# Kernel optimization log

Measured on AMD Instinct MI355X. Metric: run time of the kernel, lower is better.

The kernel has to match this reference:

```python
import jax, jax.numpy as jnp
import numpy as np

ELEM, EMBD, WIN = 128, 128, 128

def setup_inputs() -> dict:
    key = jax.random.key(0)
    ks = jax.random.split(key, 7)
    s = 1.0 / np.sqrt(ELEM)
    return {
        "x": jax.random.normal(ks[0], (8, 16384, ELEM), dtype=jnp.float32),
        "Wq": jax.random.uniform(ks[1], (EMBD, ELEM), jnp.float32, -s, s),
        "bq": jax.random.uniform(ks[2], (EMBD,), jnp.float32, -s, s),
        "Wk": jax.random.uniform(ks[3], (EMBD, ELEM), jnp.float32, -s, s),
        "bk": jax.random.uniform(ks[4], (EMBD,), jnp.float32, -s, s),
        "Wv": jax.random.uniform(ks[5], (EMBD, ELEM), jnp.float32, -s, s),
        "bv": jax.random.uniform(ks[6], (EMBD,), jnp.float32, -s, s),
    }

def reference(x, Wq, bq, Wk, bk, Wv, bv):
    N, S, E = x.shape
    P = S // WIN
    xp = x.reshape(N, P, WIN, E)  # [N,P,W,E]
    q = jnp.einsum('npwe,de->npwd', xp, Wq) + bq
    k = jnp.einsum('npwe,de->npwd', xp, Wk) + bk
    v = jnp.einsum('npwe,de->npwd', xp, Wv) + bv
    # note: original applies NO 1/sqrt(d) scaling
    scores = jnp.einsum('npwd,npud->npwu', q, k)  # [N,P,W,W]
    attn = jax.nn.softmax(scores, axis=-1)
    out = jnp.einsum('npwu,npud->npwd', attn, v)
    return out.reshape(N, S, EMBD)
```

## Files before the change

kernel.cpp:

```cpp
#include <hip/hip_runtime.h>

#define LDSP 136

typedef _Float16 h8 __attribute__((ext_vector_type(8)));
typedef _Float16 h4 __attribute__((ext_vector_type(4)));
typedef float    f4 __attribute__((ext_vector_type(4)));

__global__ void prep(const float* __restrict__ Wq, const float* __restrict__ Wk,
                     const float* __restrict__ bq, _Float16* __restrict__ Mt,
                     float* __restrict__ ck) {
    int idx = blockIdx.x * 256 + threadIdx.x;
    int e = idx & 127, f = idx >> 7;
    float a0 = 0.f, a1 = 0.f, a2 = 0.f, a3 = 0.f;
    for (int d = 0; d < 128; d += 4) {
        a0 += Wk[(d + 0) * 128 + f] * Wq[(d + 0) * 128 + e];
        a1 += Wk[(d + 1) * 128 + f] * Wq[(d + 1) * 128 + e];
        a2 += Wk[(d + 2) * 128 + f] * Wq[(d + 2) * 128 + e];
        a3 += Wk[(d + 3) * 128 + f] * Wq[(d + 3) * 128 + e];
    }
    Mt[idx] = (_Float16)((a0 + a1) + (a2 + a3));

    if (blockIdx.x == 0 && threadIdx.x < 128) {
        int t = threadIdx.x;
        float c0 = 0.f, c1 = 0.f, c2 = 0.f, c3 = 0.f;
        for (int d = 0; d < 128; d += 4) {
            c0 += bq[d + 0] * Wk[(d + 0) * 128 + t];
            c1 += bq[d + 1] * Wk[(d + 1) * 128 + t];
            c2 += bq[d + 2] * Wk[(d + 2) * 128 + t];
            c3 += bq[d + 3] * Wk[(d + 3) * 128 + t];
        }
        ck[t] = (c0 + c1) + (c2 + c3);
    }
}

__global__ __launch_bounds__(512, 2) void attn(
    const float* __restrict__ x, const _Float16* __restrict__ Mt,
    const float* __restrict__ Wv, const float* __restrict__ ck,
    const float* __restrict__ bv, float* __restrict__ out) {
    __shared__ _Float16 Xs[2][128 * LDSP];
    __shared__ _Float16 Ts[128 * LDSP];
    __shared__ _Float16 Vs[128 * LDSP];

    const int tid  = threadIdx.x;
    const int wave = tid >> 6;
    const int lane = tid & 63;
    const int quad = lane >> 4;
    const int l16  = lane & 15;
    const int wb   = wave * 16;

    h8 aT[4], aV[4];
    for (int e0 = 0; e0 < 4; ++e0) {
        aT[e0] = *(const h8*)(Mt + (wb + l16) * 128 + e0 * 32 + quad * 8);
        const float* wp = Wv + (wb + l16) * 128 + e0 * 32 + quad * 8;
        f4 w0 = *(const f4*)(wp);
        f4 w1 = *(const f4*)(wp + 4);
        aV[e0] = (h8){(_Float16)w0.x, (_Float16)w0.y, (_Float16)w0.z, (_Float16)w0.w,
                      (_Float16)w1.x, (_Float16)w1.y, (_Float16)w1.z, (_Float16)w1.w};
    }
    f4 ck4  = *(const f4*)(ck + wb + quad * 4);
    float bvv = bv[wb + l16];

    const size_t base0 = (size_t)blockIdx.x * 4 * (128 * 128);

    f4 pf[8];
    for (int j = 0; j < 8; ++j)
        pf[j] = *(const f4*)(x + base0 + 4 * tid + 2048 * j);

    for (int it = 0; it < 4; ++it) {
        _Float16* X = Xs[it & 1];

        for (int j = 0; j < 8; ++j) {
            int idx = 4 * tid + 2048 * j;
            int row = idx >> 7, col = idx & 127;
            f4 f = pf[j];
            h4 h = {(_Float16)f.x, (_Float16)f.y, (_Float16)f.z, (_Float16)f.w};
            *(h4*)(&X[row * LDSP + col]) = h;
        }
        __syncthreads();

        if (it < 3) {
            const float* nx = x + base0 + (size_t)(it + 1) * (128 * 128);
            for (int j = 0; j < 8; ++j)
                pf[j] = *(const f4*)(nx + 4 * tid + 2048 * j);
        }

        {
            f4 accT[8], accV[8];
            for (int t = 0; t < 8; ++t) {
                accT[t] = ck4;
                accV[t] = (f4){bvv, bvv, bvv, bvv};
            }
            for (int e0 = 0; e0 < 4; ++e0) {
                h8 b[8];
                for (int nt = 0; nt < 8; ++nt)
                    b[nt] = *(const h8*)(&X[(nt * 16 + l16) * LDSP + e0 * 32 + quad * 8]);
                for (int nt = 0; nt < 8; ++nt) {
                    accT[nt] = __builtin_amdgcn_mfma_f32_16x16x32_f16(aT[e0], b[nt], accT[nt], 0, 0, 0);
                    accV[nt] = __builtin_amdgcn_mfma_f32_16x16x32_f16(b[nt], aV[e0], accV[nt], 0, 0, 0);
                }
            }
            for (int nt = 0; nt < 8; ++nt) {
                f4 v = accT[nt];
                h4 h = {(_Float16)v.x, (_Float16)v.y, (_Float16)v.z, (_Float16)v.w};
                *(h4*)(&Ts[(nt * 16 + l16) * LDSP + wb + quad * 4]) = h;
                v = accV[nt];
                h4 g = {(_Float16)v.x, (_Float16)v.y, (_Float16)v.z, (_Float16)v.w};
                *(h4*)(&Vs[(wb + l16) * LDSP + nt * 16 + quad * 4]) = g;
            }
        }
        __syncthreads();

        f4 acc[8];
        for (int mt = 0; mt < 8; ++mt) acc[mt] = (f4){0.f, 0.f, 0.f, 0.f};
        for (int f0 = 0; f0 < 4; ++f0) {
            h8 bt = *(const h8*)(&Ts[(wb + l16) * LDSP + f0 * 32 + quad * 8]);
            h8 a[8];
            for (int mt = 0; mt < 8; ++mt)
                a[mt] = *(const h8*)(&X[(mt * 16 + l16) * LDSP + f0 * 32 + quad * 8]);
            for (int mt = 0; mt < 8; ++mt)
                acc[mt] = __builtin_amdgcn_mfma_f32_16x16x32_f16(a[mt], bt, acc[mt], 0, 0, 0);
        }
        {
            float m = -1e30f;
            for (int mt = 0; mt < 8; ++mt) {
                f4 v = acc[mt];
                m = fmaxf(m, fmaxf(fmaxf(v.x, v.y), fmaxf(v.z, v.w)));
            }
            m = fmaxf(m, __shfl_xor(m, 16, 64));
            m = fmaxf(m, __shfl_xor(m, 32, 64));
            float s = 0.f;
            for (int mt = 0; mt < 8; ++mt) {
                f4 v = acc[mt];
                v.x = __expf(v.x - m); v.y = __expf(v.y - m);
                v.z = __expf(v.z - m); v.w = __expf(v.w - m);
                acc[mt] = v;
                s += v.x + v.y + v.z + v.w;
            }
            s += __shfl_xor(s, 16, 64);
            s += __shfl_xor(s, 32, 64);
            float inv = 1.0f / s;
            for (int mt = 0; mt < 8; ++mt) {
                f4 v = acc[mt];
                h4 h = {(_Float16)(v.x * inv), (_Float16)(v.y * inv),
                        (_Float16)(v.z * inv), (_Float16)(v.w * inv)};
                *(h4*)(&Ts[(wb + l16) * LDSP + mt * 16 + quad * 4]) = h;
            }
        }

        for (int nt = 0; nt < 8; ++nt) acc[nt] = (f4){0.f, 0.f, 0.f, 0.f};
        for (int u0 = 0; u0 < 4; ++u0) {
            h8 ap = *(const h8*)(&Ts[(wb + l16) * LDSP + u0 * 32 + quad * 8]);
            h8 b[8];
            for (int nt = 0; nt < 8; ++nt)
                b[nt] = *(const h8*)(&Vs[(nt * 16 + l16) * LDSP + u0 * 32 + quad * 8]);
            for (int nt = 0; nt < 8; ++nt)
                acc[nt] = __builtin_amdgcn_mfma_f32_16x16x32_f16(ap, b[nt], acc[nt], 0, 0, 0);
        }
        float* ob = out + base0 + (size_t)it * (128 * 128);
        for (int nt = 0; nt < 8; ++nt) {
            f4 v = acc[nt];
            int w0 = wb + quad * 4;
            int d  = nt * 16 + l16;
            ob[(size_t)(w0 + 0) * 128 + d] = v.x;
            ob[(size_t)(w0 + 1) * 128 + d] = v.y;
            ob[(size_t)(w0 + 2) * 128 + d] = v.z;
            ob[(size_t)(w0 + 3) * 128 + d] = v.w;
        }
    }
}

extern "C" void kernel_launch(void* const* d_in, const int* in_sizes, int n_in,
                              void* d_out, int out_size, void* d_ws, size_t ws_size,
                              hipStream_t stream) {
    const float* x  = (const float*)d_in[0];
    const float* Wq = (const float*)d_in[1];
    const float* bq = (const float*)d_in[2];
    const float* Wk = (const float*)d_in[3];
    const float* Wv = (const float*)d_in[5];
    const float* bv = (const float*)d_in[6];

    _Float16* Mt  = (_Float16*)d_ws;
    float*    ckp = (float*)(Mt + 16384);

    prep<<<64, 256, 0, stream>>>(Wq, Wk, bq, Mt, ckp);
    attn<<<256, 512, 0, stream>>>(x, Mt, Wv, ckp, bv, (float*)d_out);
}
```

Before: 141.1 us.

## Switch to 32x32x16 MFMA tiles with 2x4 wave split and cross-wave softmax

Replaces the 16x16x32 MFMA decomposition with 32x32x16 MFMAs. Each wave now owns a 32-row by 64-column tile in a 4x2 wave grid, which cuts LDS fragment loads per MFMA and reuses the X fragments across the T, V and score products. Softmax is split across two waves, so row max and sum are combined through a small shared buffer with an extra barrier. X double buffering is dropped in favour of a single buffer, and the next-tile prefetch moves to after the second barrier. This adds a synchronisation point and more registers per thread.

New measurement: 144.0 us. 2.1% more time.

```diff
diff --git a/kernel.cpp b/kernel.cpp
--- a/kernel.cpp
+++ b/kernel.cpp
@@ -5,6 +5,7 @@
 typedef _Float16 h8 __attribute__((ext_vector_type(8)));
 typedef _Float16 h4 __attribute__((ext_vector_type(4)));
 typedef float    f4 __attribute__((ext_vector_type(4)));
+typedef float    fx16 __attribute__((ext_vector_type(16)));
 
 __global__ void prep(const float* __restrict__ Wq, const float* __restrict__ Wk,
                      const float* __restrict__ bq, _Float16* __restrict__ Mt,
@@ -37,134 +38,160 @@
     const float* __restrict__ x, const _Float16* __restrict__ Mt,
     const float* __restrict__ Wv, const float* __restrict__ ck,
     const float* __restrict__ bv, float* __restrict__ out) {
-    __shared__ _Float16 Xs[2][128 * LDSP];
+    __shared__ _Float16 Xs[128 * LDSP];
     __shared__ _Float16 Ts[128 * LDSP];
     __shared__ _Float16 Vs[128 * LDSP];
+    __shared__ float2   Sm[256];
 
     const int tid  = threadIdx.x;
-    const int wave = tid >> 6;
+    const int wv   = tid >> 6;
     const int lane = tid & 63;
-    const int quad = lane >> 4;
-    const int l16  = lane & 15;
-    const int wb   = wave * 16;
-
-    h8 aT[4], aV[4];
-    for (int e0 = 0; e0 < 4; ++e0) {
-        aT[e0] = *(const h8*)(Mt + (wb + l16) * 128 + e0 * 32 + quad * 8);
-        const float* wp = Wv + (wb + l16) * 128 + e0 * 32 + quad * 8;
-        f4 w0 = *(const f4*)(wp);
+    const int l32  = lane & 31;
+    const int hi   = lane >> 5;
+    const int hv   = wv & 1;
+    const int t4   = wv >> 1;
+
+    h8 mtf[8], wvf[8];
+#pragma unroll
+    for (int e0 = 0; e0 < 8; ++e0) {
+        mtf[e0] = *(const h8*)(Mt + (t4 * 32 + l32) * 128 + e0 * 16 + hi * 8);
+        const float* wp = Wv + (t4 * 32 + l32) * 128 + e0 * 16 + hi * 8;
+        f4 w0 = *(const f4*)wp;
         f4 w1 = *(const f4*)(wp + 4);
-        aV[e0] = (h8){(_Float16)w0.x, (_Float16)w0.y, (_Float16)w0.z, (_Float16)w0.w,
-                      (_Float16)w1.x, (_Float16)w1.y, (_Float16)w1.z, (_Float16)w1.w};
-    }
-    f4 ck4  = *(const f4*)(ck + wb + quad * 4);
-    float bvv = bv[wb + l16];
+        wvf[e0] = (h8){(_Float16)w0.x, (_Float16)w0.y, (_Float16)w0.z, (_Float16)w0.w,
+                       (_Float16)w1.x, (_Float16)w1.y, (_Float16)w1.z, (_Float16)w1.w};
+    }
+    const float bvv = bv[t4 * 32 + l32];
 
     const size_t base0 = (size_t)blockIdx.x * 4 * (128 * 128);
 
     f4 pf[8];
+#pragma unroll
     for (int j = 0; j < 8; ++j)
         pf[j] = *(const f4*)(x + base0 + 4 * tid + 2048 * j);
 
     for (int it = 0; it < 4; ++it) {
-        _Float16* X = Xs[it & 1];
-
+#pragma unroll
         for (int j = 0; j < 8; ++j) {
             int idx = 4 * tid + 2048 * j;
             int row = idx >> 7, col = idx & 127;
             f4 f = pf[j];
             h4 h = {(_Float16)f.x, (_Float16)f.y, (_Float16)f.z, (_Float16)f.w};
-            *(h4*)(&X[row * LDSP + col]) = h;
+            *(h4*)(&Xs[row * LDSP + col]) = h;
+        }
+        __syncthreads();
+
+        h8 xf0[8], xf1[8];
+        fx16 accT0, accT1;
+        {
+            f4 ckv[4];
+#pragma unroll
+            for (int run = 0; run < 4; ++run)
+                ckv[run] = *(const f4*)(ck + t4 * 32 + run * 8 + 4 * hi);
+#pragma unroll
+            for (int r = 0; r < 16; ++r) accT0[r] = ckv[r >> 2][r & 3];
+            accT1 = accT0;
+        }
+#pragma unroll
+        for (int e0 = 0; e0 < 8; ++e0) {
+            xf0[e0] = *(const h8*)(&Xs[(hv * 64 + l32) * LDSP + e0 * 16 + hi * 8]);
+            xf1[e0] = *(const h8*)(&Xs[(hv * 64 + 32 + l32) * LDSP + e0 * 16 + hi * 8]);
+            accT0 = __builtin_amdgcn_mfma_f32_32x32x16_f16(mtf[e0], xf0[e0], accT0, 0, 0, 0);
+            accT1 = __builtin_amdgcn_mfma_f32_32x32x16_f16(mtf[e0], xf1[e0], accT1, 0, 0, 0);
+        }
+#pragma unroll
+        for (int run = 0; run < 4; ++run) {
+            h4 h0 = {(_Float16)accT0[run * 4 + 0], (_Float16)accT0[run * 4 + 1],
+                     (_Float16)accT0[run * 4 + 2], (_Float16)accT0[run * 4 + 3]};
+            *(h4*)(&Ts[(hv * 64 + l32) * LDSP + t4 * 32 + run * 8 + 4 * hi]) = h0;
+            h4 h1 = {(_Float16)accT1[run * 4 + 0], (_Float16)accT1[run * 4 + 1],
+                     (_Float16)accT1[run * 4 + 2], (_Float16)accT1[run * 4 + 3]};
+            *(h4*)(&Ts[(hv * 64 + 32 + l32) * LDSP + t4 * 32 + run * 8 + 4 * hi]) = h1;
+        }
+
+        fx16 accV0, accV1;
+#pragma unroll
+        for (int r = 0; r < 16; ++r) accV0[r] = bvv;
+        accV1 = accV0;
+#pragma unroll
+        for (int e0 = 0; e0 < 8; ++e0) {
+            accV0 = __builtin_amdgcn_mfma_f32_32x32x16_f16(xf0[e0], wvf[e0], accV0, 0, 0, 0);
+            accV1 = __builtin_amdgcn_mfma_f32_32x32x16_f16(xf1[e0], wvf[e0], accV1, 0, 0, 0);
+        }
+#pragma unroll
+        for (int run = 0; run < 4; ++run) {
+            h4 g0 = {(_Float16)accV0[run * 4 + 0], (_Float16)accV0[run * 4 + 1],
+                     (_Float16)accV0[run * 4 + 2], (_Float16)accV0[run * 4 + 3]};
+            *(h4*)(&Vs[(t4 * 32 + l32) * LDSP + hv * 64 + run * 8 + 4 * hi]) = g0;
+            h4 g1 = {(_Float16)accV1[run * 4 + 0], (_Float16)accV1[run * 4 + 1],
+                     (_Float16)accV1[run * 4 + 2], (_Float16)accV1[run * 4 + 3]};
+            *(h4*)(&Vs[(t4 * 32 + l32) * LDSP + hv * 64 + 32 + run * 8 + 4 * hi]) = g1;
         }
         __syncthreads();
 
         if (it < 3) {
             const float* nx = x + base0 + (size_t)(it + 1) * (128 * 128);
+#pragma unroll
             for (int j = 0; j < 8; ++j)
                 pf[j] = *(const f4*)(nx + 4 * tid + 2048 * j);
         }
 
-        {
-            f4 accT[8], accV[8];
-            for (int t = 0; t < 8; ++t) {
-                accT[t] = ck4;
-                accV[t] = (f4){bvv, bvv, bvv, bvv};
-            }
-            for (int e0 = 0; e0 < 4; ++e0) {
-                h8 b[8];
-                for (int nt = 0; nt < 8; ++nt)
-                    b[nt] = *(const h8*)(&X[(nt * 16 + l16) * LDSP + e0 * 32 + quad * 8]);
-                for (int nt = 0; nt < 8; ++nt) {
-                    accT[nt] = __builtin_amdgcn_mfma_f32_16x16x32_f16(aT[e0], b[nt], accT[nt], 0, 0, 0);
-                    accV[nt] = __builtin_amdgcn_mfma_f32_16x16x32_f16(b[nt], aV[e0], accV[nt], 0, 0, 0);
-                }
-            }
-            for (int nt = 0; nt < 8; ++nt) {
-                f4 v = accT[nt];
-                h4 h = {(_Float16)v.x, (_Float16)v.y, (_Float16)v.z, (_Float16)v.w};
-                *(h4*)(&Ts[(nt * 16 + l16) * LDSP + wb + quad * 4]) = h;
-                v = accV[nt];
-                h4 g = {(_Float16)v.x, (_Float16)v.y, (_Float16)v.z, (_Float16)v.w};
-                *(h4*)(&Vs[(wb + l16) * LDSP + nt * 16 + quad * 4]) = g;
-            }
-        }
-        __syncthreads();
-
-        f4 acc[8];
-        for (int mt = 0; mt < 8; ++mt) acc[mt] = (f4){0.f, 0.f, 0.f, 0.f};
-        for (int f0 = 0; f0 < 4; ++f0) {
-            h8 bt = *(const h8*)(&Ts[(wb + l16) * LDSP + f0 * 32 + quad * 8]);
-            h8 a[8];
-            for (int mt = 0; mt < 8; ++mt)
-                a[mt] = *(const h8*)(&X[(mt * 16 + l16) * LDSP + f0 * 32 + quad * 8]);
-            for (int mt = 0; mt < 8; ++mt)
-                acc[mt] = __builtin_amdgcn_mfma_f32_16x16x32_f16(a[mt], bt, acc[mt], 0, 0, 0);
-        }
-        {
-            float m = -1e30f;
-            for (int mt = 0; mt < 8; ++mt) {
-                f4 v = acc[mt];
-                m = fmaxf(m, fmaxf(fmaxf(v.x, v.y), fmaxf(v.z, v.w)));
-            }
-            m = fmaxf(m, __shfl_xor(m, 16, 64));
-            m = fmaxf(m, __shfl_xor(m, 32, 64));
-            float s = 0.f;
-            for (int mt = 0; mt < 8; ++mt) {
-                f4 v = acc[mt];
-                v.x = __expf(v.x - m); v.y = __expf(v.y - m);
-                v.z = __expf(v.z - m); v.w = __expf(v.w - m);
-                acc[mt] = v;
-                s += v.x + v.y + v.z + v.w;
-            }
-            s += __shfl_xor(s, 16, 64);
-            s += __shfl_xor(s, 32, 64);
-            float inv = 1.0f / s;
-            for (int mt = 0; mt < 8; ++mt) {
-                f4 v = acc[mt];
-                h4 h = {(_Float16)(v.x * inv), (_Float16)(v.y * inv),
-                        (_Float16)(v.z * inv), (_Float16)(v.w * inv)};
-                *(h4*)(&Ts[(wb + l16) * LDSP + mt * 16 + quad * 4]) = h;
-            }
-        }
-
-        for (int nt = 0; nt < 8; ++nt) acc[nt] = (f4){0.f, 0.f, 0.f, 0.f};
-        for (int u0 = 0; u0 < 4; ++u0) {
-            h8 ap = *(const h8*)(&Ts[(wb + l16) * LDSP + u0 * 32 + quad * 8]);
-            h8 b[8];
-            for (int nt = 0; nt < 8; ++nt)
-                b[nt] = *(const h8*)(&Vs[(nt * 16 + l16) * LDSP + u0 * 32 + quad * 8]);
-            for (int nt = 0; nt < 8; ++nt)
-                acc[nt] = __builtin_amdgcn_mfma_f32_16x16x32_f16(ap, b[nt], acc[nt], 0, 0, 0);
+        fx16 s0, s1;
+#pragma unroll
+        for (int r = 0; r < 16; ++r) s0[r] = 0.f;
+        s1 = s0;
+#pragma unroll
+        for (int f0 = 0; f0 < 8; ++f0) {
+            h8 tf = *(const h8*)(&Ts[(t4 * 32 + l32) * LDSP + f0 * 16 + hi * 8]);
+            s0 = __builtin_amdgcn_mfma_f32_32x32x16_f16(xf0[f0], tf, s0, 0, 0, 0);
+            s1 = __builtin_amdgcn_mfma_f32_32x32x16_f16(xf1[f0], tf, s1, 0, 0, 0);
+        }
+        float m = -1e30f;
+#pragma unroll
+        for (int r = 0; r < 16; ++r) m = fmaxf(m, fmaxf(s0[r], s1[r]));
+        m = fmaxf(m, __shfl_xor(m, 32, 64));
+        float ss = 0.f;
+#pragma unroll
+        for (int r = 0; r < 16; ++r) {
+            s0[r] = __expf(s0[r] - m);
+            s1[r] = __expf(s1[r] - m);
+            ss += s0[r] + s1[r];
+        }
+        ss += __shfl_xor(ss, 32, 64);
+        if (hi == 0) Sm[hv * 128 + t4 * 32 + l32] = make_float2(m, ss);
+        __syncthreads();
+        float2 om = Sm[(hv ^ 1) * 128 + t4 * 32 + l32];
+        float M   = fmaxf(m, om.x);
+        float inv = __expf(m - M) / (ss * __expf(m - M) + om.y * __expf(om.x - M));
+#pragma unroll
+        for (int run = 0; run < 4; ++run) {
+            h4 p0 = {(_Float16)(s0[run * 4 + 0] * inv), (_Float16)(s0[run * 4 + 1] * inv),
+                     (_Float16)(s0[run * 4 + 2] * inv), (_Float16)(s0[run * 4 + 3] * inv)};
+            *(h4*)(&Ts[(t4 * 32 + l32) * LDSP + hv * 64 + run * 8 + 4 * hi]) = p0;
+            h4 p1 = {(_Float16)(s1[run * 4 + 0] * inv), (_Float16)(s1[run * 4 + 1] * inv),
+                     (_Float16)(s1[run * 4 + 2] * inv), (_Float16)(s1[run * 4 + 3] * inv)};
+            *(h4*)(&Ts[(t4 * 32 + l32) * LDSP + hv * 64 + 32 + run * 8 + 4 * hi]) = p1;
+        }
+        __syncthreads();
+
+        fx16 o0, o1;
+#pragma unroll
+        for (int r = 0; r < 16; ++r) o0[r] = 0.f;
+        o1 = o0;
+#pragma unroll
+        for (int u0 = 0; u0 < 8; ++u0) {
+            h8 pr = *(const h8*)(&Ts[(t4 * 32 + l32) * LDSP + u0 * 16 + hi * 8]);
+            h8 v0 = *(const h8*)(&Vs[(hv * 64 + l32) * LDSP + u0 * 16 + hi * 8]);
+            h8 v1 = *(const h8*)(&Vs[(hv * 64 + 32 + l32) * LDSP + u0 * 16 + hi * 8]);
+            o0 = __builtin_amdgcn_mfma_f32_32x32x16_f16(pr, v0, o0, 0, 0, 0);
+            o1 = __builtin_amdgcn_mfma_f32_32x32x16_f16(pr, v1, o1, 0, 0, 0);
         }
         float* ob = out + base0 + (size_t)it * (128 * 128);
-        for (int nt = 0; nt < 8; ++nt) {
-            f4 v = acc[nt];
-            int w0 = wb + quad * 4;
-            int d  = nt * 16 + l16;
-            ob[(size_t)(w0 + 0) * 128 + d] = v.x;
-            ob[(size_t)(w0 + 1) * 128 + d] = v.y;
-            ob[(size_t)(w0 + 2) * 128 + d] = v.z;
-            ob[(size_t)(w0 + 3) * 128 + d] = v.w;
+#pragma unroll
+        for (int r = 0; r < 16; ++r) {
+            int w = t4 * 32 + (r & 3) + 8 * (r >> 2) + 4 * hi;
+            ob[(size_t)w * 128 + hv * 64 + l32]      = o0[r];
+            ob[(size_t)w * 128 + hv * 64 + 32 + l32] = o1[r];
         }
     }
 }
```
